# Performance work log

Hardware: AMD Instinct MI355X
Metric: run time of the kernel (lower is better)

Reference implementation:

```python
import jax, jax.numpy as jnp
import numpy as np

MAX_NUM_CENTERS = 100
CENTER_IGNORE_PX = 3
SIGMA = 2.0   # center_gt_blur
KSIZE = 21    # GaussianLayer kernel size (ReflectionPad2d(10) + Conv2d(k=21))


def _gauss_kernel():
    r = KSIZE // 2
    x = jnp.arange(-r, r + 1, dtype=jnp.float32)
    g = jnp.exp(-0.5 * (x / SIGMA) ** 2)
    g = g / g.sum()
    return jnp.outer(g, g)  # [21,21], sums to 1 (matches scipy gaussian_filter of a delta)


def _gaussian_blur(x):
    # x: [B,H,W] -> depthwise 21x21 gaussian with reflect padding (GaussianLayer)
    r = KSIZE // 2
    k = _gauss_kernel()[None, None]  # [1,1,21,21]
    xp = jnp.pad(x[:, None], ((0, 0), (0, 0), (r, r), (r, r)), mode="reflect")
    y = jax.lax.conv_general_dilated(xp, k, (1, 1), "VALID",
                                     dimension_numbers=("NCHW", "OIHW", "NCHW"))
    return y[:, 0]


def setup_inputs() -> dict:
    key = jax.random.key(0)
    k1, k2 = jax.random.split(key)
    B, H, W = 8, 768, 768
    instances = jax.random.randint(k1, (B, 1, H, W), 0, MAX_NUM_CENTERS, dtype=jnp.int32)
    centers = jax.random.uniform(k2, (B, MAX_NUM_CENTERS, 2), dtype=jnp.float32) * (H - 1) + 1.0
    return {"instances": instances, "centers": centers}


def reference(instances, centers):
    B, _, H, W = instances.shape
    inst = instances[:, 0]                                # [B,H,W]
    col = jnp.arange(W, dtype=jnp.float32)                # xym_s[0][i,j] = j
    row = jnp.arange(H, dtype=jnp.float32)[:, None]       # xym_s[1][i,j] = i

    valid = inst > 0                                      # instance_mask
    has_inst = jnp.any(valid, axis=(1, 2)).astype(jnp.float32)  # len(unique)>1 gate

    # per-pixel nearest-center gather: center = centers[b, id-1]
    idx = jnp.clip(inst - 1, 0, MAX_NUM_CENTERS - 1)
    c = centers[jnp.arange(B)[:, None, None], idx]        # [B,H,W,2]
    gt_cx = jnp.where(valid, c[..., 1], -10000.0)         # gt_center_x (swapped coords)
    gt_cy = jnp.where(valid, c[..., 0], -10000.0)

    gt_X = gt_cx - row                                    # gt_center_x - xym_s[1]
    gt_Y = gt_cy - col                                    # gt_center_y - xym_s[0]

    near = (jnp.abs(gt_X) < CENTER_IGNORE_PX) & (jnp.abs(gt_Y) < CENTER_IGNORE_PX)
    # batches with no instances skip the block -> ignore stays all-ones
    ignore = jnp.where(has_inst[:, None, None] > 0, (~near).astype(jnp.float32), 1.0)

    m = valid.astype(jnp.float32)
    R = jnp.sqrt(gt_X ** 2 + gt_Y ** 2) * m
    theta_raw = jnp.arctan2(gt_Y, gt_X)
    theta = theta_raw * has_inst[:, None, None]           # skipped (zero) when no instances
    s = jnp.sin(theta_raw) * m
    cth = jnp.cos(theta_raw) * m
    M = jnp.sqrt(s ** 2 + cth ** 2)                       # == m, kept for faithfulness
    s = jnp.where(valid, s / jnp.maximum(M, 1e-12), 0.0)
    cth = jnp.where(valid, cth / jnp.maximum(M, 1e-12), 0.0)

    # gt_center_mask: zeros if no center-neighborhood pixels, else normalized blur
    blur = _gaussian_blur(1.0 - ignore)
    all_ones = jnp.all(ignore >= 1.0, axis=(1, 2))        # gt_center_mask.all()
    bmax = jnp.max(blur, axis=(1, 2), keepdims=True)
    cmask = jnp.where(all_ones[:, None, None], 0.0, blur / jnp.maximum(bmax, 1e-12))

    top = jnp.stack([R, theta, s, cth, ignore, cmask], axis=1)       # [B,6,H,W]
    mat = jnp.concatenate([top, jnp.zeros((B, 7, H, W), top.dtype)], axis=1)[:, :, None]
    # mat: [B,13,1,H,W]; channels 6..12 are zero (no orientation input)

    # gt_centers[id] = centers[b, id-1][[1,0]] for each instance id present
    present = jnp.zeros((B, MAX_NUM_CENTERS), dtype=bool).at[
        jnp.arange(B)[:, None], inst.reshape(B, -1)].set(True)
    swapped = centers[..., ::-1]
    gt_centers = jnp.zeros_like(centers).at[:, 1:, :].set(
        jnp.where(present[:, 1:, None], swapped[:, :-1, :], 0.0))

    return mat, gt_centers
```

## Files before the change

kernel.cpp:

```cpp
#include <hip/hip_runtime.h>
#include <math.h>

#define NB 8
#define NH 768
#define NW 768
#define NHW (NH*NW)
#define NCEN 100
#define NPIX (NB*NHW)
#define RAD 10
#define KS 21

#define SCAN_BLKS (NPIX / 4096)
#define BLKS_PER_B (NHW / 4096)
#define CAND_BLKS 96
#define NPQ 3
#define FBLK_PX (NPQ*1024)
#define QBLK3_PER_B (NHW / FBLK_PX)
#define BSLOT 24
#define BCAP 23
#define GCAP 256
#define FCAP 256

#define STORE(v, p) (*(p) = (v))

#define OFF_MASKS 0
#define OFF_BLIST 4608
#define OFF_BMAXP 32256
#define OFF_HAS   33024
#define OFF_M     33032
#define OFF_GLIST 33040

typedef float f4 __attribute__((ext_vector_type(4)));

__device__ const float g_G[KS] = {
    7.4335e-7f, 7.9919e-6f, 6.6915e-5f, 0.00043634f, 0.00221592f,
    0.00876415f, 0.02699548f, 0.06475880f, 0.12098536f, 0.17603266f,
    0.19947114f,
    0.17603266f, 0.12098536f, 0.06475880f, 0.02699548f, 0.00876415f,
    0.00221592f, 0.00043634f, 6.6915e-5f, 7.9919e-6f, 7.4335e-7f};

__device__ __forceinline__ float wfun(int p, int q, const float* __restrict__ g) {
    int d = p - q;
    float w = 0.f;
    if (d >= -RAD && d <= RAD) w = g[d + RAD];
    int a = p + q;
    if (q > 0 && a <= RAD) w += g[a + RAD];
    if (q < NH - 1 && a >= 2 * (NH - 1) - RAD) w += g[a - 2 * (NH - 1) + RAD];
    return w;
}

__device__ __forceinline__ float fatan2(float Y, float X) {
    float ax = fabsf(X), ay = fabsf(Y);
    float mx = fmaxf(ax, ay), mn = fminf(ax, ay);
    float a = mx > 0.f ? __fdividef(mn, mx) : 0.f;
    float ss = a * a;
    float r = fmaf(fmaf(fmaf(fmaf(fmaf(-0.01172120f, ss, 0.05265332f), ss,
                -0.11643287f), ss, 0.19354346f), ss, -0.33262347f), ss, 0.99997726f) * a;
    if (ay > ax) r = 1.57079637f - r;
    if (X < 0.f) r = 3.14159274f - r;
    return copysignf(r, Y);
}

__global__ __launch_bounds__(256) void k_main(const int4* __restrict__ inst4,
                                              const float* __restrict__ centers,
                                              int* __restrict__ ws,
                                              float* __restrict__ out) {
    __shared__ unsigned sm[4];
    __shared__ float2 s_c2[NCEN];
    __shared__ int s_loc[BCAP];
    __shared__ int s_lcnt;
    int t = threadIdx.x;
    int blk = blockIdx.x;
    int b = blk / BLKS_PER_B;
    int lblk = blk - b * BLKS_PER_B;
    if (t < 4) sm[t] = 0;
    if (t == 0) s_lcnt = 0;
    for (int k = t; k < NCEN; k += 256)
        s_c2[k] = ((const float2*)centers)[b * NCEN + k];
    __syncthreads();

    unsigned m0 = 0, m1 = 0, m2 = 0, m3 = 0;
    size_t base = (size_t)blk * 1024 + t;
    int ppb = lblk * 4096 + t * 4;
    float* outb = out + (size_t)b * 13 * NHW;
    const f4 z = {0.f, 0.f, 0.f, 0.f};
#pragma unroll
    for (int q = 0; q < 4; q++) {
        int4 v = inst4[base + (size_t)q * 256];
        int pp = ppb + q * 1024;
        int gi = pp / NW;
        int gj0 = pp - gi * NW;
        int ia[4] = {v.x, v.y, v.z, v.w};
        f4 vR, vTh, vS, vC, vIg;
#pragma unroll
        for (int e = 0; e < 4; e++) {
            int iv = ia[e];
            bool valid = iv > 0;
            if (valid) {
                unsigned bit = 1u << (iv & 31);
                int w = iv >> 5;
                if (w == 0) m0 |= bit; else if (w == 1) m1 |= bit;
                else if (w == 2) m2 |= bit; else m3 |= bit;
            }
            int idx = iv - 1;
            idx = idx < 0 ? 0 : (idx > NCEN - 1 ? NCEN - 1 : idx);
            float2 c = s_c2[idx];
            float gcx = valid ? c.y : -10000.f;
            float gcy = valid ? c.x : -10000.f;
            float X = gcx - (float)gi;
            float Y = gcy - (float)(gj0 + e);
            bool near = (fabsf(X) < 3.f) && (fabsf(Y) < 3.f);
            if (valid && near) {
                int slot = atomicAdd(&s_lcnt, 1);
                if (slot < BCAP) s_loc[slot] = (gi << 16) | (gj0 + e);
            }
            vIg[e] = near ? 0.f : 1.f;
            float m = valid ? 1.f : 0.f;
            float R2 = X * X + Y * Y;
            vR[e] = sqrtf(R2) * m;
            float rinv = R2 > 0.f ? rsqrtf(R2) : 0.f;
            vS[e] = valid ? Y * rinv : 0.f;
            vC[e] = valid ? (R2 > 0.f ? X * rinv : 1.f) : 0.f;
            vTh[e] = fatan2(Y, X);
        }
        STORE(vR,  (f4*)&outb[(size_t)0 * NHW + pp]);
        STORE(vTh, (f4*)&outb[(size_t)1 * NHW + pp]);
        STORE(vS,  (f4*)&outb[(size_t)2 * NHW + pp]);
        STORE(vC,  (f4*)&outb[(size_t)3 * NHW + pp]);
        STORE(vIg, (f4*)&outb[(size_t)4 * NHW + pp]);
#pragma unroll
        for (int ch = 6; ch < 13; ++ch)
            STORE(z, (f4*)&outb[(size_t)ch * NHW + pp]);
    }
#pragma unroll
    for (int off = 32; off >= 1; off >>= 1) {
        m0 |= __shfl_xor(m0, off);
        m1 |= __shfl_xor(m1, off);
        m2 |= __shfl_xor(m2, off);
        m3 |= __shfl_xor(m3, off);
    }
    if ((t & 63) == 0) {
        if (m0) atomicOr(&sm[0], m0);
        if (m1) atomicOr(&sm[1], m1);
        if (m2) atomicOr(&sm[2], m2);
        if (m3) atomicOr(&sm[3], m3);
    }
    __syncthreads();
    if (t < 4) ws[OFF_MASKS + blk * 4 + t] = (int)sm[t];
    int cnt = s_lcnt < BCAP ? s_lcnt : BCAP;
    int* slot = &ws[OFF_BLIST + blk * BSLOT];
    if (t == 0) slot[0] = cnt;
    if (t < cnt) slot[1 + t] = s_loc[t];
}

__global__ __launch_bounds__(256) void k_bmax(const float* __restrict__ centers,
                                              int* __restrict__ ws,
                                              float* __restrict__ out) {
    __shared__ float s_g[KS];
    __shared__ int s_list[GCAP];
    __shared__ int s_tot;
    __shared__ unsigned s_m[4];
    __shared__ float s_red[4];
    int t = threadIdx.x;
    int b = blockIdx.x / CAND_BLKS;
    int cb = blockIdx.x - b * CAND_BLKS;
    if (t < KS) s_g[t] = g_G[t];
    if (t == 0) s_tot = 0;
    if (t < 4) s_m[t] = 0;
    __syncthreads();
    if (t < BLKS_PER_B) {
        const int* slot = &ws[OFF_BLIST + (b * BLKS_PER_B + t) * BSLOT];
        int cnt = slot[0];
        cnt = cnt < 0 ? 0 : (cnt > BCAP ? BCAP : cnt);
        int basep = atomicAdd(&s_tot, cnt);
        for (int i2 = 0; i2 < cnt; i2++) {
            int s = basep + i2;
            if (s < GCAP) s_list[s] = slot[1 + i2];
        }
        if (cb == 0) {
            const unsigned* pm = (const unsigned*)&ws[OFF_MASKS + (b * BLKS_PER_B + t) * 4];
            unsigned w0 = pm[0], w1 = pm[1], w2 = pm[2], w3 = pm[3];
            if (w0) atomicOr(&s_m[0], w0);
            if (w1) atomicOr(&s_m[1], w1);
            if (w2) atomicOr(&s_m[2], w2);
            if (w3) atomicOr(&s_m[3], w3);
        }
    }
    __syncthreads();
    int M = s_tot < GCAP ? s_tot : GCAP;

    if (cb == 0) {
        float* gt = out + (size_t)NB * 13 * NHW;
        if (t < NCEN) {
            float vx = 0.f, vy = 0.f;
            if (t >= 1 && ((s_m[t >> 5] >> (t & 31)) & 1u)) {
                vx = centers[(b * NCEN + (t - 1)) * 2 + 1];
                vy = centers[(b * NCEN + (t - 1)) * 2 + 0];
            }
            gt[(b * NCEN + t) * 2 + 0] = vx;
            gt[(b * NCEN + t) * 2 + 1] = vy;
        }
        if (t == 0) {
            unsigned any = (s_m[0] & 0xFFFFFFFEu) | s_m[1] | s_m[2] | s_m[3];
            ws[OFF_HAS + b] = any ? 1 : 0;
            ws[OFF_M + b] = M;
        }
        for (int e = t; e < M; e += 256) ws[OFF_GLIST + b * GCAP + e] = s_list[e];
    }

    float lmax = 0.f;
    int total = M * (KS * KS);
    for (int c = cb * 256 + t; c < total; c += CAND_BLKS * 256) {
        int m = c / (KS * KS), r = c - m * (KS * KS);
        int e = s_list[m];
        int pi = (e >> 16) + r / KS - RAD;
        int pj = (e & 0xFFFF) + (r - (r / KS) * KS) - RAD;
        if (pi < 0 || pi >= NH || pj < 0 || pj >= NW) continue;
        float acc = 0.f;
        for (int m2 = 0; m2 < M; m2++) {
            int e2 = s_list[m2];
            float wi = wfun(pi, e2 >> 16, s_g);
            if (wi == 0.f) continue;
            acc += wi * wfun(pj, e2 & 0xFFFF, s_g);
        }
        lmax = fmaxf(lmax, acc);
    }
#pragma unroll
    for (int off = 32; off >= 1; off >>= 1) lmax = fmaxf(lmax, __shfl_down(lmax, off));
    if ((t & 63) == 0) s_red[t >> 6] = lmax;
    __syncthreads();
    if (t == 0) {
        float bmx = fmaxf(fmaxf(s_red[0], s_red[1]), fmaxf(s_red[2], s_red[3]));
        ((float*)ws)[OFF_BMAXP + b * CAND_BLKS + cb] = bmx;
    }
}

__global__ __launch_bounds__(256) void k_cmask(const int* __restrict__ ws,
                                               float* __restrict__ out) {
    __shared__ float s_g[KS];
    __shared__ int s_fl[FCAP];
    __shared__ int s_fM;
    __shared__ unsigned s_bm;
    int t = threadIdx.x;
    int b = blockIdx.x / QBLK3_PER_B;
    int qblk = blockIdx.x - b * QBLK3_PER_B;

    int has = ws[OFF_HAS + b];
    int M = ws[OFF_M + b];
    if (t < KS) s_g[t] = g_G[t];
    if (t == 255) s_fM = 0;
    if (t == 254) s_bm = 0;
    __syncthreads();

    if (t < CAND_BLKS)
        atomicMax(&s_bm, __float_as_uint(((const float*)ws)[OFF_BMAXP + b * CAND_BLKS + t]));

    int p0blk = qblk * FBLK_PX;
    int r0 = qblk * 4;
    const int* gl = &ws[OFF_GLIST + b * GCAP];
    for (int m = t; m < M; m += 256) {
        int e = gl[m];
        int qi = e >> 16;
        bool keep = false;
#pragma unroll
        for (int rr = 0; rr < 4; rr++) keep |= (wfun(r0 + rr, qi, s_g) != 0.f);
        if (keep) {
            int slot = atomicAdd(&s_fM, 1);
            if (slot < FCAP) s_fl[slot] = e;
        }
    }
    __syncthreads();
    int FM = s_fM < FCAP ? s_fM : FCAP;
    float bmx = __uint_as_float(s_bm);
    float sc = (has && M > 0) ? 1.f / fmaxf(bmx, 1e-12f) : 0.f;

    float* outb = out + (size_t)b * 13 * NHW;
    const f4 z = {0.f, 0.f, 0.f, 0.f};
    for (int qq = 0; qq < NPQ; ++qq) {
        int p0 = p0blk + qq * 1024 + t * 4;
        int gi = p0 / NW;
        int gj0 = p0 - gi * NW;
        f4 blur = {0.f, 0.f, 0.f, 0.f};
        for (int m = 0; m < FM; m++) {
            int e2 = s_fl[m];
            float wi = wfun(gi, e2 >> 16, s_g);
            if (wi == 0.f) continue;
            int qj = e2 & 0xFFFF;
#pragma unroll
            for (int e = 0; e < 4; e++) blur[e] += wi * wfun(gj0 + e, qj, s_g);
        }
        f4 vCm = blur * sc;
        STORE(vCm, (f4*)&outb[(size_t)5 * NHW + p0]);
        if (!has)
            STORE(z, (f4*)&outb[(size_t)1 * NHW + p0]);
    }
}

extern "C" void kernel_launch(void* const* d_in, const int* in_sizes, int n_in,
                              void* d_out, int out_size, void* d_ws, size_t ws_size,
                              hipStream_t stream) {
    const int* inst = (const int*)d_in[0];
    const float* centers = (const float*)d_in[1];
    float* out = (float*)d_out;
    int* ws = (int*)d_ws;

    k_main<<<SCAN_BLKS, 256, 0, stream>>>((const int4*)inst, centers, ws, out);
    k_bmax<<<NB * CAND_BLKS, 256, 0, stream>>>(centers, ws, out);
    k_cmask<<<NB * QBLK3_PER_B, 256, 0, stream>>>(ws, out);
}
```

Measured before the change: 294.7 us.

## Fuse three kernels into one cooperative kernel with grid syncs

Replaces the scan, block-max and cmask kernels with a single cooperative kernel of 1152 blocks that uses grid.sync between phases. Per-pixel instance ids are packed into registers so the input is not re-read. All per-pixel outputs (R, theta, s, cth, ignore, cmask) are written once in the final phase instead of theta being rewritten later, and the zero channels are spread across all blocks in the middle phase. The aim is to remove launch gaps and redundant traffic, at the cost of grid-wide barriers and an occupancy limit of 5 blocks per CU needed for co-residency. A three-kernel fallback is used when cooperative launch is unavailable.

```diff
diff --git a/kernel.cpp b/kernel.cpp
--- a/kernel.cpp
+++ b/kernel.cpp
@@ -1,5 +1,8 @@
 #include <hip/hip_runtime.h>
+#include <hip/hip_cooperative_groups.h>
 #include <math.h>
+
+namespace cg = cooperative_groups;
 
 #define NB 8
 #define NH 768
@@ -13,9 +16,8 @@
 #define SCAN_BLKS (NPIX / 4096)
 #define BLKS_PER_B (NHW / 4096)
 #define CAND_BLKS 96
-#define NPQ 3
-#define FBLK_PX (NPQ*1024)
-#define QBLK3_PER_B (NHW / FBLK_PX)
+#define ZPB 7168
+#define ZIT (ZPB/256)
 #define BSLOT 24
 #define BCAP 23
 #define GCAP 256
@@ -61,59 +63,216 @@
     return copysignf(r, Y);
 }
 
-__global__ __launch_bounds__(256) void k_main(const int4* __restrict__ inst4,
-                                              const float* __restrict__ centers,
-                                              int* __restrict__ ws,
-                                              float* __restrict__ out) {
+__global__ __launch_bounds__(256, 5) void k_coop(const int4* __restrict__ inst4,
+                                                 const float* __restrict__ centers,
+                                                 int* __restrict__ ws,
+                                                 float* __restrict__ out) {
+    __shared__ float2 s_c2[NCEN];
+    __shared__ float s_g[KS];
     __shared__ unsigned sm[4];
-    __shared__ float2 s_c2[NCEN];
     __shared__ int s_loc[BCAP];
     __shared__ int s_lcnt;
+    __shared__ int s_list[GCAP];
+    __shared__ int s_tot;
+    __shared__ float s_red[4];
+    __shared__ int s_fl[FCAP];
+    __shared__ int s_fM;
+    __shared__ unsigned s_bm;
+
+    cg::grid_group grid = cg::this_grid();
     int t = threadIdx.x;
     int blk = blockIdx.x;
     int b = blk / BLKS_PER_B;
     int lblk = blk - b * BLKS_PER_B;
+
     if (t < 4) sm[t] = 0;
     if (t == 0) s_lcnt = 0;
+    if (t < KS) s_g[t] = g_G[t];
     for (int k = t; k < NCEN; k += 256)
         s_c2[k] = ((const float2*)centers)[b * NCEN + k];
     __syncthreads();
 
     unsigned m0 = 0, m1 = 0, m2 = 0, m3 = 0;
+    unsigned pk[4];
     size_t base = (size_t)blk * 1024 + t;
     int ppb = lblk * 4096 + t * 4;
-    float* outb = out + (size_t)b * 13 * NHW;
-    const f4 z = {0.f, 0.f, 0.f, 0.f};
 #pragma unroll
     for (int q = 0; q < 4; q++) {
         int4 v = inst4[base + (size_t)q * 256];
+        pk[q] = ((unsigned)v.x & 255u) | (((unsigned)v.y & 255u) << 8) |
+                (((unsigned)v.z & 255u) << 16) | (((unsigned)v.w & 255u) << 24);
         int pp = ppb + q * 1024;
-        int gi = pp / NW;
-        int gj0 = pp - gi * NW;
-        int ia[4] = {v.x, v.y, v.z, v.w};
-        f4 vR, vTh, vS, vC, vIg;
+        int i = pp / NW;
+        int j0 = pp - i * NW;
+        int a[4] = {v.x, v.y, v.z, v.w};
 #pragma unroll
         for (int e = 0; e < 4; e++) {
-            int iv = ia[e];
-            bool valid = iv > 0;
-            if (valid) {
+            int iv = a[e];
+            if (iv > 0) {
                 unsigned bit = 1u << (iv & 31);
                 int w = iv >> 5;
                 if (w == 0) m0 |= bit; else if (w == 1) m1 |= bit;
                 else if (w == 2) m2 |= bit; else m3 |= bit;
-            }
+                int idx = iv - 1;
+                idx = idx > NCEN - 1 ? NCEN - 1 : idx;
+                float2 c = s_c2[idx];
+                if (fabsf(c.y - (float)i) < 3.f && fabsf(c.x - (float)(j0 + e)) < 3.f) {
+                    int slot = atomicAdd(&s_lcnt, 1);
+                    if (slot < BCAP) s_loc[slot] = (i << 16) | (j0 + e);
+                }
+            }
+        }
+    }
+#pragma unroll
+    for (int off = 32; off >= 1; off >>= 1) {
+        m0 |= __shfl_xor(m0, off);
+        m1 |= __shfl_xor(m1, off);
+        m2 |= __shfl_xor(m2, off);
+        m3 |= __shfl_xor(m3, off);
+    }
+    if ((t & 63) == 0) {
+        if (m0) atomicOr(&sm[0], m0);
+        if (m1) atomicOr(&sm[1], m1);
+        if (m2) atomicOr(&sm[2], m2);
+        if (m3) atomicOr(&sm[3], m3);
+    }
+    __syncthreads();
+    if (t < 4) ws[OFF_MASKS + blk * 4 + t] = (int)sm[t];
+    {
+        int cnt = s_lcnt < BCAP ? s_lcnt : BCAP;
+        int* slot = &ws[OFF_BLIST + blk * BSLOT];
+        if (t == 0) slot[0] = cnt;
+        if (t < cnt) slot[1 + t] = s_loc[t];
+    }
+    __threadfence();
+    grid.sync();
+
+    if (blk < NB * CAND_BLKS) {
+        int b2 = blk / CAND_BLKS;
+        int cb = blk - b2 * CAND_BLKS;
+        if (t == 0) s_tot = 0;
+        if (t < 4) sm[t] = 0;
+        __syncthreads();
+        if (t < BLKS_PER_B) {
+            const int* slot = &ws[OFF_BLIST + (b2 * BLKS_PER_B + t) * BSLOT];
+            int cnt = slot[0];
+            cnt = cnt < 0 ? 0 : (cnt > BCAP ? BCAP : cnt);
+            int basep = atomicAdd(&s_tot, cnt);
+            for (int i2 = 0; i2 < cnt; i2++) {
+                int s = basep + i2;
+                if (s < GCAP) s_list[s] = slot[1 + i2];
+            }
+            if (cb == 0) {
+                const unsigned* pm = (const unsigned*)&ws[OFF_MASKS + (b2 * BLKS_PER_B + t) * 4];
+                unsigned w0 = pm[0], w1 = pm[1], w2 = pm[2], w3 = pm[3];
+                if (w0) atomicOr(&sm[0], w0);
+                if (w1) atomicOr(&sm[1], w1);
+                if (w2) atomicOr(&sm[2], w2);
+                if (w3) atomicOr(&sm[3], w3);
+            }
+        }
+        __syncthreads();
+        int M = s_tot < GCAP ? s_tot : GCAP;
+
+        if (cb == 0) {
+            float* gt = out + (size_t)NB * 13 * NHW;
+            if (t < NCEN) {
+                float vx = 0.f, vy = 0.f;
+                if (t >= 1 && ((sm[t >> 5] >> (t & 31)) & 1u)) {
+                    vx = centers[(b2 * NCEN + (t - 1)) * 2 + 1];
+                    vy = centers[(b2 * NCEN + (t - 1)) * 2 + 0];
+                }
+                gt[(b2 * NCEN + t) * 2 + 0] = vx;
+                gt[(b2 * NCEN + t) * 2 + 1] = vy;
+            }
+            if (t == 0) {
+                unsigned any = (sm[0] & 0xFFFFFFFEu) | sm[1] | sm[2] | sm[3];
+                ws[OFF_HAS + b2] = any ? 1 : 0;
+                ws[OFF_M + b2] = M;
+            }
+            for (int e = t; e < M; e += 256) ws[OFF_GLIST + b2 * GCAP + e] = s_list[e];
+        }
+
+        float lmax = 0.f;
+        int total = M * (KS * KS);
+        for (int c = blk * 256 - b2 * CAND_BLKS * 256 + t; c < total; c += CAND_BLKS * 256) {
+            int m = c / (KS * KS), r = c - m * (KS * KS);
+            int e = s_list[m];
+            int pi = (e >> 16) + r / KS - RAD;
+            int pj = (e & 0xFFFF) + (r - (r / KS) * KS) - RAD;
+            if (pi < 0 || pi >= NH || pj < 0 || pj >= NW) continue;
+            float acc = 0.f;
+            for (int m2 = 0; m2 < M; m2++) {
+                int e2 = s_list[m2];
+                float wi = wfun(pi, e2 >> 16, s_g);
+                if (wi == 0.f) continue;
+                acc += wi * wfun(pj, e2 & 0xFFFF, s_g);
+            }
+            lmax = fmaxf(lmax, acc);
+        }
+#pragma unroll
+        for (int off = 32; off >= 1; off >>= 1) lmax = fmaxf(lmax, __shfl_down(lmax, off));
+        if ((t & 63) == 0) s_red[t >> 6] = lmax;
+        __syncthreads();
+        if (t == 0) {
+            float bmx = fmaxf(fmaxf(s_red[0], s_red[1]), fmaxf(s_red[2], s_red[3]));
+            ((float*)ws)[OFF_BMAXP + b2 * CAND_BLKS + blk - b2 * CAND_BLKS] = bmx;
+        }
+    }
+    {
+        const f4 z = {0.f, 0.f, 0.f, 0.f};
+        int rem0 = lblk * ZPB;
+        f4* dst = (f4*)(out + (size_t)b * 13 * NHW + (size_t)6 * NHW) + rem0 + t;
+#pragma unroll
+        for (int it = 0; it < ZIT; ++it) STORE(z, dst + it * 256);
+    }
+    __threadfence();
+    grid.sync();
+
+    if (t == 255) s_fM = 0;
+    if (t == 254) s_bm = 0;
+    __syncthreads();
+    int has = ws[OFF_HAS + b];
+    int M3 = ws[OFF_M + b];
+    if (t < CAND_BLKS)
+        atomicMax(&s_bm, __float_as_uint(((const float*)ws)[OFF_BMAXP + b * CAND_BLKS + t]));
+    int pp0 = lblk * 4096;
+    int ri0 = pp0 / NW, ri1 = (pp0 + 4095) / NW;
+    const int* gl = &ws[OFF_GLIST + b * GCAP];
+    for (int m = t; m < M3; m += 256) {
+        int e = gl[m];
+        int qi = e >> 16;
+        if (qi >= ri0 - RAD && qi <= ri1 + RAD) {
+            int slot = atomicAdd(&s_fM, 1);
+            if (slot < FCAP) s_fl[slot] = e;
+        }
+    }
+    __syncthreads();
+    int FM = s_fM < FCAP ? s_fM : FCAP;
+    float sc = (has && M3 > 0) ? 1.f / fmaxf(__uint_as_float(s_bm), 1e-12f) : 0.f;
+    float* outb = out + (size_t)b * 13 * NHW;
+
+#pragma unroll
+    for (int q = 0; q < 4; q++) {
+        int pp = ppb + q * 1024;
+        int gi = pp / NW;
+        int gj0 = pp - gi * NW;
+        unsigned v8 = pk[q];
+        int ia[4] = {(int)(v8 & 255u), (int)((v8 >> 8) & 255u),
+                     (int)((v8 >> 16) & 255u), (int)(v8 >> 24)};
+        f4 vR, vTh, vS, vC, vIg;
+#pragma unroll
+        for (int e = 0; e < 4; e++) {
+            int iv = ia[e];
+            bool valid = iv > 0;
             int idx = iv - 1;
-            idx = idx < 0 ? 0 : (idx > NCEN - 1 ? NCEN - 1 : idx);
+            idx = idx < 0 ? 0 : idx;
             float2 c = s_c2[idx];
             float gcx = valid ? c.y : -10000.f;
             float gcy = valid ? c.x : -10000.f;
             float X = gcx - (float)gi;
             float Y = gcy - (float)(gj0 + e);
             bool near = (fabsf(X) < 3.f) && (fabsf(Y) < 3.f);
-            if (valid && near) {
-                int slot = atomicAdd(&s_lcnt, 1);
-                if (slot < BCAP) s_loc[slot] = (gi << 16) | (gj0 + e);
-            }
             vIg[e] = near ? 0.f : 1.f;
             float m = valid ? 1.f : 0.f;
             float R2 = X * X + Y * Y;
@@ -121,165 +280,8 @@
             float rinv = R2 > 0.f ? rsqrtf(R2) : 0.f;
             vS[e] = valid ? Y * rinv : 0.f;
             vC[e] = valid ? (R2 > 0.f ? X * rinv : 1.f) : 0.f;
-            vTh[e] = fatan2(Y, X);
-        }
-        STORE(vR,  (f4*)&outb[(size_t)0 * NHW + pp]);
-        STORE(vTh, (f4*)&outb[(size_t)1 * NHW + pp]);
-        STORE(vS,  (f4*)&outb[(size_t)2 * NHW + pp]);
-        STORE(vC,  (f4*)&outb[(size_t)3 * NHW + pp]);
-        STORE(vIg, (f4*)&outb[(size_t)4 * NHW + pp]);
-#pragma unroll
-        for (int ch = 6; ch < 13; ++ch)
-            STORE(z, (f4*)&outb[(size_t)ch * NHW + pp]);
-    }
-#pragma unroll
-    for (int off = 32; off >= 1; off >>= 1) {
-        m0 |= __shfl_xor(m0, off);
-        m1 |= __shfl_xor(m1, off);
-        m2 |= __shfl_xor(m2, off);
-        m3 |= __shfl_xor(m3, off);
-    }
-    if ((t & 63) == 0) {
-        if (m0) atomicOr(&sm[0], m0);
-        if (m1) atomicOr(&sm[1], m1);
-        if (m2) atomicOr(&sm[2], m2);
-        if (m3) atomicOr(&sm[3], m3);
-    }
-    __syncthreads();
-    if (t < 4) ws[OFF_MASKS + blk * 4 + t] = (int)sm[t];
-    int cnt = s_lcnt < BCAP ? s_lcnt : BCAP;
-    int* slot = &ws[OFF_BLIST + blk * BSLOT];
-    if (t == 0) slot[0] = cnt;
-    if (t < cnt) slot[1 + t] = s_loc[t];
-}
-
-__global__ __launch_bounds__(256) void k_bmax(const float* __restrict__ centers,
-                                              int* __restrict__ ws,
-                                              float* __restrict__ out) {
-    __shared__ float s_g[KS];
-    __shared__ int s_list[GCAP];
-    __shared__ int s_tot;
-    __shared__ unsigned s_m[4];
-    __shared__ float s_red[4];
-    int t = threadIdx.x;
-    int b = blockIdx.x / CAND_BLKS;
-    int cb = blockIdx.x - b * CAND_BLKS;
-    if (t < KS) s_g[t] = g_G[t];
-    if (t == 0) s_tot = 0;
-    if (t < 4) s_m[t] = 0;
-    __syncthreads();
-    if (t < BLKS_PER_B) {
-        const int* slot = &ws[OFF_BLIST + (b * BLKS_PER_B + t) * BSLOT];
-        int cnt = slot[0];
-        cnt = cnt < 0 ? 0 : (cnt > BCAP ? BCAP : cnt);
-        int basep = atomicAdd(&s_tot, cnt);
-        for (int i2 = 0; i2 < cnt; i2++) {
-            int s = basep + i2;
-            if (s < GCAP) s_list[s] = slot[1 + i2];
-        }
-        if (cb == 0) {
-            const unsigned* pm = (const unsigned*)&ws[OFF_MASKS + (b * BLKS_PER_B + t) * 4];
-            unsigned w0 = pm[0], w1 = pm[1], w2 = pm[2], w3 = pm[3];
-            if (w0) atomicOr(&s_m[0], w0);
-            if (w1) atomicOr(&s_m[1], w1);
-            if (w2) atomicOr(&s_m[2], w2);
-            if (w3) atomicOr(&s_m[3], w3);
-        }
-    }
-    __syncthreads();
-    int M = s_tot < GCAP ? s_tot : GCAP;
-
-    if (cb == 0) {
-        float* gt = out + (size_t)NB * 13 * NHW;
-        if (t < NCEN) {
-            float vx = 0.f, vy = 0.f;
-            if (t >= 1 && ((s_m[t >> 5] >> (t & 31)) & 1u)) {
-                vx = centers[(b * NCEN + (t - 1)) * 2 + 1];
-                vy = centers[(b * NCEN + (t - 1)) * 2 + 0];
-            }
-            gt[(b * NCEN + t) * 2 + 0] = vx;
-            gt[(b * NCEN + t) * 2 + 1] = vy;
-        }
-        if (t == 0) {
-            unsigned any = (s_m[0] & 0xFFFFFFFEu) | s_m[1] | s_m[2] | s_m[3];
-            ws[OFF_HAS + b] = any ? 1 : 0;
-            ws[OFF_M + b] = M;
-        }
-        for (int e = t; e < M; e += 256) ws[OFF_GLIST + b * GCAP + e] = s_list[e];
-    }
-
-    float lmax = 0.f;
-    int total = M * (KS * KS);
-    for (int c = cb * 256 + t; c < total; c += CAND_BLKS * 256) {
-        int m = c / (KS * KS), r = c - m * (KS * KS);
-        int e = s_list[m];
-        int pi = (e >> 16) + r / KS - RAD;
-        int pj = (e & 0xFFFF) + (r - (r / KS) * KS) - RAD;
-        if (pi < 0 || pi >= NH || pj < 0 || pj >= NW) continue;
-        float acc = 0.f;
-        for (int m2 = 0; m2 < M; m2++) {
-            int e2 = s_list[m2];
-            float wi = wfun(pi, e2 >> 16, s_g);
-            if (wi == 0.f) continue;
-            acc += wi * wfun(pj, e2 & 0xFFFF, s_g);
-        }
-        lmax = fmaxf(lmax, acc);
-    }
-#pragma unroll
-    for (int off = 32; off >= 1; off >>= 1) lmax = fmaxf(lmax, __shfl_down(lmax, off));
-    if ((t & 63) == 0) s_red[t >> 6] = lmax;
-    __syncthreads();
-    if (t == 0) {
-        float bmx = fmaxf(fmaxf(s_red[0], s_red[1]), fmaxf(s_red[2], s_red[3]));
-        ((float*)ws)[OFF_BMAXP + b * CAND_BLKS + cb] = bmx;
-    }
-}
-
-__global__ __launch_bounds__(256) void k_cmask(const int* __restrict__ ws,
-                                               float* __restrict__ out) {
-    __shared__ float s_g[KS];
-    __shared__ int s_fl[FCAP];
-    __shared__ int s_fM;
-    __shared__ unsigned s_bm;
-    int t = threadIdx.x;
-    int b = blockIdx.x / QBLK3_PER_B;
-    int qblk = blockIdx.x - b * QBLK3_PER_B;
-
-    int has = ws[OFF_HAS + b];
-    int M = ws[OFF_M + b];
-    if (t < KS) s_g[t] = g_G[t];
-    if (t == 255) s_fM = 0;
-    if (t == 254) s_bm = 0;
-    __syncthreads();
-
-    if (t < CAND_BLKS)
-        atomicMax(&s_bm, __float_as_uint(((const float*)ws)[OFF_BMAXP + b * CAND_BLKS + t]));
-
-    int p0blk = qblk * FBLK_PX;
-    int r0 = qblk * 4;
-    const int* gl = &ws[OFF_GLIST + b * GCAP];
-    for (int m = t; m < M; m += 256) {
-        int e = gl[m];
-        int qi = e >> 16;
-        bool keep = false;
-#pragma unroll
-        for (int rr = 0; rr < 4; rr++) keep |= (wfun(r0 + rr, qi, s_g) != 0.f);
-        if (keep) {
-            int slot = atomicAdd(&s_fM, 1);
-            if (slot < FCAP) s_fl[slot] = e;
-        }
-    }
-    __syncthreads();
-    int FM = s_fM < FCAP ? s_fM : FCAP;
-    float bmx = __uint_as_float(s_bm);
-    float sc = (has && M > 0) ? 1.f / fmaxf(bmx, 1e-12f) : 0.f;
-
-    float* outb = out + (size_t)b * 13 * NHW;
-    const f4 z = {0.f, 0.f, 0.f, 0.f};
-    for (int qq = 0; qq < NPQ; ++qq) {
-        int p0 = p0blk + qq * 1024 + t * 4;
-        int gi = p0 / NW;
-        int gj0 = p0 - gi * NW;
+            vTh[e] = has ? fatan2(Y, X) : 0.f;
+        }
         f4 blur = {0.f, 0.f, 0.f, 0.f};
         for (int m = 0; m < FM; m++) {
             int e2 = s_fl[m];
@@ -290,9 +292,240 @@
             for (int e = 0; e < 4; e++) blur[e] += wi * wfun(gj0 + e, qj, s_g);
         }
         f4 vCm = blur * sc;
+        STORE(vR,  (f4*)&outb[(size_t)0 * NHW + pp]);
+        STORE(vTh, (f4*)&outb[(size_t)1 * NHW + pp]);
+        STORE(vS,  (f4*)&outb[(size_t)2 * NHW + pp]);
+        STORE(vC,  (f4*)&outb[(size_t)3 * NHW + pp]);
+        STORE(vIg, (f4*)&outb[(size_t)4 * NHW + pp]);
+        STORE(vCm, (f4*)&outb[(size_t)5 * NHW + pp]);
+    }
+}
+
+__global__ __launch_bounds__(256) void k_scan_fb(const int4* __restrict__ inst4,
+                                                 const float* __restrict__ centers,
+                                                 int* __restrict__ ws) {
+    __shared__ unsigned sm[4];
+    __shared__ float2 s_c2[NCEN];
+    __shared__ int s_loc[BCAP];
+    __shared__ int s_lcnt;
+    int t = threadIdx.x, blk = blockIdx.x;
+    int b = blk / BLKS_PER_B, lblk = blk - b * BLKS_PER_B;
+    if (t < 4) sm[t] = 0;
+    if (t == 0) s_lcnt = 0;
+    for (int k = t; k < NCEN; k += 256)
+        s_c2[k] = ((const float2*)centers)[b * NCEN + k];
+    __syncthreads();
+    unsigned m0 = 0, m1 = 0, m2 = 0, m3 = 0;
+    size_t base = (size_t)blk * 1024 + t;
+    int ppb = lblk * 4096 + t * 4;
+#pragma unroll
+    for (int q = 0; q < 4; q++) {
+        int4 v = inst4[base + (size_t)q * 256];
+        int pp = ppb + q * 1024;
+        int i = pp / NW, j0 = pp - (pp / NW) * NW;
+        int a[4] = {v.x, v.y, v.z, v.w};
+#pragma unroll
+        for (int e = 0; e < 4; e++) {
+            int iv = a[e];
+            if (iv > 0) {
+                unsigned bit = 1u << (iv & 31);
+                int w = iv >> 5;
+                if (w == 0) m0 |= bit; else if (w == 1) m1 |= bit;
+                else if (w == 2) m2 |= bit; else m3 |= bit;
+                int idx = iv - 1;
+                idx = idx > NCEN - 1 ? NCEN - 1 : idx;
+                float2 c = s_c2[idx];
+                if (fabsf(c.y - (float)i) < 3.f && fabsf(c.x - (float)(j0 + e)) < 3.f) {
+                    int slot = atomicAdd(&s_lcnt, 1);
+                    if (slot < BCAP) s_loc[slot] = (i << 16) | (j0 + e);
+                }
+            }
+        }
+    }
+#pragma unroll
+    for (int off = 32; off >= 1; off >>= 1) {
+        m0 |= __shfl_xor(m0, off); m1 |= __shfl_xor(m1, off);
+        m2 |= __shfl_xor(m2, off); m3 |= __shfl_xor(m3, off);
+    }
+    if ((t & 63) == 0) {
+        if (m0) atomicOr(&sm[0], m0);
+        if (m1) atomicOr(&sm[1], m1);
+        if (m2) atomicOr(&sm[2], m2);
+        if (m3) atomicOr(&sm[3], m3);
+    }
+    __syncthreads();
+    if (t < 4) ws[OFF_MASKS + blk * 4 + t] = (int)sm[t];
+    int cnt = s_lcnt < BCAP ? s_lcnt : BCAP;
+    int* slot = &ws[OFF_BLIST + blk * BSLOT];
+    if (t == 0) slot[0] = cnt;
+    if (t < cnt) slot[1 + t] = s_loc[t];
+}
+
+__global__ __launch_bounds__(256) void k_mid_fb(const float* __restrict__ centers,
+                                                int* __restrict__ ws,
+                                                float* __restrict__ out) {
+    int t = threadIdx.x, g = blockIdx.x;
+    if (g < NB * CAND_BLKS) {
+        __shared__ float s_g[KS];
+        __shared__ int s_list[GCAP];
+        __shared__ int s_tot;
+        __shared__ unsigned s_m[4];
+        __shared__ float s_red[4];
+        int b = g / CAND_BLKS, cb = g - b * CAND_BLKS;
+        if (t < KS) s_g[t] = g_G[t];
+        if (t == 0) s_tot = 0;
+        if (t < 4) s_m[t] = 0;
+        __syncthreads();
+        if (t < BLKS_PER_B) {
+            const int* slot = &ws[OFF_BLIST + (b * BLKS_PER_B + t) * BSLOT];
+            int cnt = slot[0];
+            cnt = cnt < 0 ? 0 : (cnt > BCAP ? BCAP : cnt);
+            int basep = atomicAdd(&s_tot, cnt);
+            for (int i2 = 0; i2 < cnt; i2++) {
+                int s = basep + i2;
+                if (s < GCAP) s_list[s] = slot[1 + i2];
+            }
+            if (cb == 0) {
+                const unsigned* pm = (const unsigned*)&ws[OFF_MASKS + (b * BLKS_PER_B + t) * 4];
+                if (pm[0]) atomicOr(&s_m[0], pm[0]);
+                if (pm[1]) atomicOr(&s_m[1], pm[1]);
+                if (pm[2]) atomicOr(&s_m[2], pm[2]);
+                if (pm[3]) atomicOr(&s_m[3], pm[3]);
+            }
+        }
+        __syncthreads();
+        int M = s_tot < GCAP ? s_tot : GCAP;
+        if (cb == 0) {
+            float* gt = out + (size_t)NB * 13 * NHW;
+            if (t < NCEN) {
+                float vx = 0.f, vy = 0.f;
+                if (t >= 1 && ((s_m[t >> 5] >> (t & 31)) & 1u)) {
+                    vx = centers[(b * NCEN + (t - 1)) * 2 + 1];
+                    vy = centers[(b * NCEN + (t - 1)) * 2 + 0];
+                }
+                gt[(b * NCEN + t) * 2 + 0] = vx;
+                gt[(b * NCEN + t) * 2 + 1] = vy;
+            }
+            if (t == 0) {
+                unsigned any = (s_m[0] & 0xFFFFFFFEu) | s_m[1] | s_m[2] | s_m[3];
+                ws[OFF_HAS + b] = any ? 1 : 0;
+                ws[OFF_M + b] = M;
+            }
+            for (int e = t; e < M; e += 256) ws[OFF_GLIST + b * GCAP + e] = s_list[e];
+        }
+        float lmax = 0.f;
+        int total = M * (KS * KS);
+        for (int c = cb * 256 + t; c < total; c += CAND_BLKS * 256) {
+            int m = c / (KS * KS), r = c - m * (KS * KS);
+            int e = s_list[m];
+            int pi = (e >> 16) + r / KS - RAD;
+            int pj = (e & 0xFFFF) + (r - (r / KS) * KS) - RAD;
+            if (pi < 0 || pi >= NH || pj < 0 || pj >= NW) continue;
+            float acc = 0.f;
+            for (int m2 = 0; m2 < M; m2++) {
+                int e2 = s_list[m2];
+                float wi = wfun(pi, e2 >> 16, s_g);
+                if (wi == 0.f) continue;
+                acc += wi * wfun(pj, e2 & 0xFFFF, s_g);
+            }
+            lmax = fmaxf(lmax, acc);
+        }
+#pragma unroll
+        for (int off = 32; off >= 1; off >>= 1) lmax = fmaxf(lmax, __shfl_down(lmax, off));
+        if ((t & 63) == 0) s_red[t >> 6] = lmax;
+        __syncthreads();
+        if (t == 0) {
+            float bmx = fmaxf(fmaxf(s_red[0], s_red[1]), fmaxf(s_red[2], s_red[3]));
+            ((float*)ws)[OFF_BMAXP + b * CAND_BLKS + cb] = bmx;
+        }
+    } else {
+        int zblk = g - NB * CAND_BLKS;
+        int b2 = zblk / 168;
+        int rem0 = (zblk - b2 * 168) * 6144;
+        const f4 z = {0.f, 0.f, 0.f, 0.f};
+        f4* dst = (f4*)out + (size_t)b2 * (13 * NHW / 4) + (6 * NHW / 4) + rem0 + t;
+#pragma unroll
+        for (int it = 0; it < 24; ++it) STORE(z, dst + it * 256);
+    }
+}
+
+__global__ __launch_bounds__(256) void k_fused_fb(const int* __restrict__ inst,
+                                                  const float* __restrict__ centers,
+                                                  const int* __restrict__ ws,
+                                                  float* __restrict__ out) {
+    __shared__ float s_cen[2 * NCEN];
+    __shared__ float s_g[KS];
+    __shared__ int s_fl[FCAP];
+    __shared__ int s_fM;
+    __shared__ unsigned s_bm;
+    int t = threadIdx.x;
+    int b = blockIdx.x / (NHW / 3072);
+    int qblk = blockIdx.x - b * (NHW / 3072);
+    int has = ws[OFF_HAS + b];
+    int M = ws[OFF_M + b];
+    for (int k = t; k < 2 * NCEN; k += 256) s_cen[k] = centers[b * 2 * NCEN + k];
+    if (t < KS) s_g[t] = g_G[t];
+    if (t == 255) s_fM = 0;
+    if (t == 254) s_bm = 0;
+    __syncthreads();
+    if (t < CAND_BLKS)
+        atomicMax(&s_bm, __float_as_uint(((const float*)ws)[OFF_BMAXP + b * CAND_BLKS + t]));
+    int p0blk = qblk * 3072;
+    int r0 = qblk * 4;
+    const int* gl = &ws[OFF_GLIST + b * GCAP];
+    for (int m = t; m < M; m += 256) {
+        int e = gl[m];
+        int qi = e >> 16;
+        if (qi >= r0 - RAD && qi <= r0 + 3 + RAD) {
+            int slot = atomicAdd(&s_fM, 1);
+            if (slot < FCAP) s_fl[slot] = e;
+        }
+    }
+    __syncthreads();
+    int FM = s_fM < FCAP ? s_fM : FCAP;
+    float sc = (has && M > 0) ? 1.f / fmaxf(__uint_as_float(s_bm), 1e-12f) : 0.f;
+    float* outb = out + (size_t)b * 13 * NHW;
+    for (int qq = 0; qq < 3; ++qq) {
+        int p0 = p0blk + qq * 1024 + t * 4;
+        int gi = p0 / NW, gj0 = p0 - (p0 / NW) * NW;
+        int4 ivv = *(const int4*)&inst[(size_t)b * NHW + p0];
+        int ia[4] = {ivv.x, ivv.y, ivv.z, ivv.w};
+        f4 vR, vTh, vS, vC, vIg;
+#pragma unroll
+        for (int e = 0; e < 4; e++) {
+            int iv = ia[e];
+            bool valid = iv > 0;
+            int idx = iv - 1;
+            idx = idx < 0 ? 0 : idx;
+            float cy = s_cen[2 * idx], cx = s_cen[2 * idx + 1];
+            float X = (valid ? cx : -10000.f) - (float)gi;
+            float Y = (valid ? cy : -10000.f) - (float)(gj0 + e);
+            bool near = (fabsf(X) < 3.f) && (fabsf(Y) < 3.f);
+            vIg[e] = near ? 0.f : 1.f;
+            float m = valid ? 1.f : 0.f;
+            float R2 = X * X + Y * Y;
+            vR[e] = sqrtf(R2) * m;
+            float rinv = R2 > 0.f ? rsqrtf(R2) : 0.f;
+            vS[e] = valid ? Y * rinv : 0.f;
+            vC[e] = valid ? (R2 > 0.f ? X * rinv : 1.f) : 0.f;
+            vTh[e] = has ? fatan2(Y, X) : 0.f;
+        }
+        f4 blur = {0.f, 0.f, 0.f, 0.f};
+        for (int m = 0; m < FM; m++) {
+            int e2 = s_fl[m];
+            float wi = wfun(gi, e2 >> 16, s_g);
+            if (wi == 0.f) continue;
+            int qj = e2 & 0xFFFF;
+#pragma unroll
+            for (int e = 0; e < 4; e++) blur[e] += wi * wfun(gj0 + e, qj, s_g);
+        }
+        f4 vCm = blur * sc;
+        STORE(vR,  (f4*)&outb[(size_t)0 * NHW + p0]);
+        STORE(vTh, (f4*)&outb[(size_t)1 * NHW + p0]);
+        STORE(vS,  (f4*)&outb[(size_t)2 * NHW + p0]);
+        STORE(vC,  (f4*)&outb[(size_t)3 * NHW + p0]);
+        STORE(vIg, (f4*)&outb[(size_t)4 * NHW + p0]);
         STORE(vCm, (f4*)&outb[(size_t)5 * NHW + p0]);
-        if (!has)
-            STORE(z, (f4*)&outb[(size_t)1 * NHW + p0]);
     }
 }
 
@@ -304,7 +537,23 @@
     float* out = (float*)d_out;
     int* ws = (int*)d_ws;
 
-    k_main<<<SCAN_BLKS, 256, 0, stream>>>((const int4*)inst, centers, ws, out);
-    k_bmax<<<NB * CAND_BLKS, 256, 0, stream>>>(centers, ws, out);
-    k_cmask<<<NB * QBLK3_PER_B, 256, 0, stream>>>(ws, out);
-}
+    static int coop = -1;
+    if (coop < 0) {
+        int dev = 0, v = 0;
+        hipGetDevice(&dev);
+        hipDeviceGetAttribute(&v, hipDeviceAttributeCooperativeLaunch, dev);
+        coop = v ? 1 : 0;
+    }
+    if (coop) {
+        const int4* inst4 = (const int4*)inst;
+        void* args[] = {(void*)&inst4, (void*)&centers, (void*)&ws, (void*)&out};
+        hipError_t err = hipLaunchCooperativeKernel((const void*)k_coop,
+                                                    dim3(SCAN_BLKS), dim3(256),
+                                                    args, 0, stream);
+        if (err == hipSuccess) return;
+        coop = 0;
+    }
+    k_scan_fb<<<SCAN_BLKS, 256, 0, stream>>>((const int4*)inst, centers, ws);
+    k_mid_fb<<<NB * CAND_BLKS + 1344, 256, 0, stream>>>(centers, ws, out);
+    k_fused_fb<<<NB * (NHW / 3072), 256, 0, stream>>>(inst, centers, ws, out);
+}
```

After: 270.3 us. -8.3%, faster.
